# Optimization experiments

Measured on AMD Instinct MI355X. Metric: run time of the kernel, lower is better.

## Reference

```python
import jax, jax.numpy as jnp
import numpy as np

B, T, C_EMBD, C_ATT = 16, 1024, 2048, 2048


def wkv(time_decay, time_first, k, v):
    """Numerically-stable RWKV WKV recurrence (matches wkv_cuda).
    time_decay/time_first: [C]; k, v: [B, T, C] -> y: [B, T, C]."""
    w = -jnp.exp(time_decay)  # [C], decay is -exp(param)
    u = time_first
    Bn, Tn, Cn = k.shape

    def step(carry, kv_t):
        aa, bb, pp = carry          # each [B, C]
        kt, vt = kv_t               # [B, C]
        ww = u + kt
        p = jnp.maximum(pp, ww)
        e1 = jnp.exp(pp - p)
        e2 = jnp.exp(ww - p)
        y = (e1 * aa + e2 * vt) / (e1 * bb + e2)
        ww2 = pp + w
        p2 = jnp.maximum(ww2, kt)
        e1b = jnp.exp(ww2 - p2)
        e2b = jnp.exp(kt - p2)
        new = (e1b * aa + e2b * vt, e1b * bb + e2b, p2)
        return new, y

    init = (jnp.zeros((Bn, Cn), k.dtype),
            jnp.zeros((Bn, Cn), k.dtype),
            jnp.full((Bn, Cn), -1e38, k.dtype))
    kT = jnp.swapaxes(k, 0, 1)  # [T, B, C]
    vT = jnp.swapaxes(v, 0, 1)
    _, ys = jax.lax.scan(step, init, (kT, vT))
    return jnp.swapaxes(ys, 0, 1)  # [B, T, C]


def setup_inputs() -> dict:
    key = jax.random.key(0)
    ks = jax.random.split(key, 10)
    xav = np.sqrt(2.0 / (C_EMBD + C_ATT))
    inp = {
        "x": jax.random.normal(ks[0], (B, T, C_EMBD), jnp.float32),
        "time_decay": jax.random.normal(ks[1], (C_ATT,), jnp.float32) * 0.02,
        "time_first": jax.random.normal(ks[2], (C_ATT,), jnp.float32) * 0.02,
        "time_mix_k": jax.random.normal(ks[3], (1, 1, C_EMBD), jnp.float32) * 0.02,
        "time_mix_v": jax.random.normal(ks[4], (1, 1, C_EMBD), jnp.float32) * 0.02,
        "time_mix_r": jax.random.normal(ks[5], (1, 1, C_EMBD), jnp.float32) * 0.02,
        "key_w": jax.random.normal(ks[6], (C_ATT, C_EMBD), jnp.float32) * xav,
        "value_w": jax.random.normal(ks[7], (C_ATT, C_EMBD), jnp.float32) * xav,
        "receptance_w": jax.random.normal(ks[8], (C_ATT, C_EMBD), jnp.float32) * xav,
        "output_w": jax.random.normal(ks[9], (C_EMBD, C_ATT), jnp.float32) * xav,
    }
    return inp


def reference(x, time_decay, time_first, time_mix_k, time_mix_v, time_mix_r,
              key_w, value_w, receptance_w, output_w):
    # time shift: xx[:, t] = x[:, t-1], xx[:, 0] = 0
    xx = jnp.pad(x, ((0, 0), (1, 0), (0, 0)))[:, :-1]
    xk = x * time_mix_k + xx * (1 - time_mix_k)
    xv = x * time_mix_v + xx * (1 - time_mix_v)
    xr = x * time_mix_r + xx * (1 - time_mix_r)
    k = jnp.einsum('btc,dc->btd', xk, key_w)
    v = jnp.einsum('btc,dc->btd', xv, value_w)
    r = jnp.einsum('btc,dc->btd', xr, receptance_w)
    sr = jax.nn.sigmoid(r)
    rwkv = sr * wkv(time_decay, time_first, k, v)
    return jnp.einsum('btd,cd->btc', rwkv, output_w)
```

## Files before the change

### kernel.cpp

```cpp
#include <hip/hip_runtime.h>
#include <hip/hip_bf16.h>

#define BB 16
#define TT 1024
#define CC 2048
#define TS 32

typedef __attribute__((ext_vector_type(4))) float f32x4;
typedef __attribute__((ext_vector_type(8))) short bf16x8;

__device__ __forceinline__ unsigned short f2bf(float f) {
  union { float f; unsigned u; } x; x.f = f;
  unsigned r = x.u + 0x7fffu + ((x.u >> 16) & 1u);
  return (unsigned short)(r >> 16);
}
__device__ __forceinline__ float bf2f(unsigned short u) {
  union { unsigned u; float f; } x; x.u = ((unsigned)u) << 16;
  return x.f;
}

__device__ __forceinline__ ushort4 mix4(float4 a, float4 b, float4 m) {
  ushort4 o;
  o.x = f2bf(a.x * m.x + b.x * (1.f - m.x));
  o.y = f2bf(a.y * m.y + b.y * (1.f - m.y));
  o.z = f2bf(a.z * m.z + b.z * (1.f - m.z));
  o.w = f2bf(a.w * m.w + b.w * (1.f - m.w));
  return o;
}

__global__ void f2bf_all(const float* __restrict__ w0, const float* __restrict__ w1,
                         const float* __restrict__ w2, const float* __restrict__ w3,
                         unsigned short* __restrict__ o0, unsigned short* __restrict__ o1,
                         unsigned short* __restrict__ o2, unsigned short* __restrict__ o3,
                         int n4each) {
  const float* ws[4] = {w0, w1, w2, w3};
  unsigned short* os[4] = {o0, o1, o2, o3};
  int total = 4 * n4each;
  for (int i = blockIdx.x * blockDim.x + threadIdx.x; i < total;
       i += gridDim.x * blockDim.x) {
    int seg = i / n4each, j = i - seg * n4each;
    float4 v = ((const float4*)ws[seg])[j];
    ushort4 o;
    o.x = f2bf(v.x); o.y = f2bf(v.y); o.z = f2bf(v.z); o.w = f2bf(v.w);
    ((ushort4*)os[seg])[j] = o;
  }
}

__global__ void mix_kernel(const float* __restrict__ x,
                           const float* __restrict__ tmk,
                           const float* __restrict__ tmv,
                           const float* __restrict__ tmr,
                           unsigned short* __restrict__ xk,
                           unsigned short* __restrict__ xv,
                           unsigned short* __restrict__ xr,
                           int t0, int Tc) {
  const int C4 = CC / 4;
  const int total = BB * Tc * C4;
  for (int g = blockIdx.x * blockDim.x + threadIdx.x; g < total;
       g += gridDim.x * blockDim.x) {
    int cg = g % C4;
    int lrow = g / C4;
    int tl = lrow % Tc;
    int b = lrow / Tc;
    int t = t0 + tl;
    size_t gidx = (size_t)(b * TT + t) * C4 + cg;
    float4 xc = ((const float4*)x)[gidx];
    float4 xp = make_float4(0.f, 0.f, 0.f, 0.f);
    if (t > 0) xp = ((const float4*)x)[gidx - C4];
    ((ushort4*)xk)[g] = mix4(xc, xp, ((const float4*)tmk)[cg]);
    ((ushort4*)xv)[g] = mix4(xc, xp, ((const float4*)tmv)[cg]);
    ((ushort4*)xr)[g] = mix4(xc, xp, ((const float4*)tmr)[cg]);
  }
}

template<bool BF16OUT>
__global__ __launch_bounds__(512, 2)
void gemm256(const unsigned short* __restrict__ A,
             const unsigned short* __restrict__ B,
             void* __restrict__ Cv, int M, int N, int K,
             int tcShift, int t0) {
  __shared__ __align__(1024) unsigned char lds[131072];
  const int tid = threadIdx.x;
  const int lane = tid & 63;
  const int wid = tid >> 6;
  const int wr = wid >> 2;
  const int wc = wid & 3;

  const int nwg = gridDim.x;
  const int cpx = nwg >> 3;
  const int bid = blockIdx.x;
  const int wg = (bid & 7) * cpx + (bid >> 3);
  const int bcolN = N >> 8;
  const int brow = wg / bcolN;
  const int bcol = wg % bcolN;

  const unsigned short* Ag = A + (size_t)(brow * 256) * K;
  const unsigned short* Bg = B + (size_t)(bcol * 256) * K;

  const int srow = tid >> 3;
  const int scolB = ((tid & 7) * 16) ^ ((srow & 7) << 4);
  const int scolE = scolB >> 1;
  const int ldsWave = wid * 1024;

#define STAGE(gbase, rowOff, ldsOff, kOff)                                     \
  __builtin_amdgcn_global_load_lds(                                            \
      (const __attribute__((address_space(1))) void*)(                         \
          (gbase) + (size_t)((rowOff) + srow) * K + (kOff) + scolE),           \
      (__attribute__((address_space(3))) void*)(lds + (ldsOff) + ldsWave),     \
      16, 0, 0)

  const int frow = lane & 15;
  const int fhi = (lane >> 4) << 4;

#define FRAG(tb, row, kk)                                                      \
  (*(const bf16x8*)(lds + (tb) + (row) * 128 +                                 \
                    ((((kk) << 6) + fhi) ^ (((row) & 7) << 4))))

#define FENCE asm volatile("" ::: "memory")

  const int NT = K >> 6;

  STAGE(Bg,   0, 32768 +     0, 0);
  STAGE(Bg,  64, 32768 +  8192, 0);
  STAGE(Bg, 128, 32768 + 16384, 0);
  STAGE(Bg, 192, 32768 + 24576, 0);
  STAGE(Ag,   0,             0, 0);
  STAGE(Ag, 128,         16384, 0);
  STAGE(Ag,  64,          8192, 0);
  STAGE(Ag, 192,         24576, 0);

  f32x4 acc[8][4] = {};
  bf16x8 af0[8], af1[8], bf0[4], bf1[4];

  asm volatile("s_waitcnt vmcnt(2)" ::: "memory");
  __builtin_amdgcn_s_barrier();
#pragma unroll
  for (int m = 0; m < 4; ++m)
#pragma unroll
    for (int kk = 0; kk < 2; ++kk)
      af0[m * 2 + kk] = FRAG(0, wr * 128 + m * 16 + frow, kk);
#pragma unroll
  for (int n = 0; n < 2; ++n)
#pragma unroll
    for (int kk = 0; kk < 2; ++kk)
      bf0[n * 2 + kk] = FRAG(32768, wc * 64 + n * 16 + frow, kk);

  for (int kt = 0; kt < NT; ++kt) {
    const int cur = (kt & 1) << 16;
    const int nxt = ((kt + 1) & 1) << 16;
    const int kN = (kt + 1) << 6;
    const bool st = (kt + 1 < NT);

    if (st) { STAGE(Bg, 0, nxt + 32768, kN); STAGE(Bg, 64, nxt + 32768 + 8192, kN); }
    __builtin_amdgcn_s_setprio(1);
#pragma unroll
    for (int m = 0; m < 4; ++m)
#pragma unroll
      for (int n = 0; n < 2; ++n)
#pragma unroll
        for (int kk = 0; kk < 2; ++kk)
          acc[m][n] = __builtin_amdgcn_mfma_f32_16x16x32_bf16(
              af0[m * 2 + kk], bf0[n * 2 + kk], acc[m][n], 0, 0, 0);
    __builtin_amdgcn_s_setprio(0);
#pragma unroll
    for (int n = 0; n < 2; ++n)
#pragma unroll
      for (int kk = 0; kk < 2; ++kk)
        bf1[n * 2 + kk] = FRAG(cur + 32768, wc * 64 + 32 + n * 16 + frow, kk);
    FENCE;
    if (st) { asm volatile("s_waitcnt vmcnt(2)" ::: "memory"); }
    else    { asm volatile("s_waitcnt vmcnt(0)" ::: "memory"); }
    __builtin_amdgcn_s_barrier();

    if (st) { STAGE(Bg, 128, nxt + 32768 + 16384, kN); STAGE(Bg, 192, nxt + 32768 + 24576, kN); }
#pragma unroll
    for (int m = 0; m < 4; ++m)
#pragma unroll
      for (int kk = 0; kk < 2; ++kk)
        af1[m * 2 + kk] = FRAG(cur, wr * 128 + 64 + m * 16 + frow, kk);
    __builtin_amdgcn_s_setprio(1);
#pragma unroll
    for (int m = 0; m < 4; ++m)
#pragma unroll
      for (int n = 0; n < 2; ++n)
#pragma unroll
        for (int kk = 0; kk < 2; ++kk)
          acc[m][2 + n] = __builtin_amdgcn_mfma_f32_16x16x32_bf16(
              af0[m * 2 + kk], bf1[n * 2 + kk], acc[m][2 + n], 0, 0, 0);
    __builtin_amdgcn_s_setprio(0);
    FENCE;
    __builtin_amdgcn_s_barrier();

    if (st) { STAGE(Ag, 0, nxt, kN); STAGE(Ag, 128, nxt + 16384, kN); }
    __builtin_amdgcn_s_setprio(1);
#pragma unroll
    for (int m = 0; m < 4; ++m)
#pragma unroll
      for (int n = 0; n < 2; ++n)
#pragma unroll
        for (int kk = 0; kk < 2; ++kk)
          acc[4 + m][2 + n] = __builtin_amdgcn_mfma_f32_16x16x32_bf16(
              af1[m * 2 + kk], bf1[n * 2 + kk], acc[4 + m][2 + n], 0, 0, 0);
    __builtin_amdgcn_s_setprio(0);
    FENCE;
    __builtin_amdgcn_s_barrier();

    if (st) { STAGE(Ag, 64, nxt + 8192, kN); STAGE(Ag, 192, nxt + 24576, kN); }
    __builtin_amdgcn_s_setprio(1);
#pragma unroll
    for (int m = 0; m < 4; ++m)
#pragma unroll
      for (int n = 0; n < 2; ++n)
#pragma unroll
        for (int kk = 0; kk < 2; ++kk)
          acc[4 + m][n] = __builtin_amdgcn_mfma_f32_16x16x32_bf16(
              af1[m * 2 + kk], bf0[n * 2 + kk], acc[4 + m][n], 0, 0, 0);
    __builtin_amdgcn_s_setprio(0);
    if (st) {
      asm volatile("s_waitcnt vmcnt(2)" ::: "memory");
      __builtin_amdgcn_s_barrier();
#pragma unroll
      for (int m = 0; m < 4; ++m)
#pragma unroll
        for (int kk = 0; kk < 2; ++kk)
          af0[m * 2 + kk] = FRAG(nxt, wr * 128 + m * 16 + frow, kk);
#pragma unroll
      for (int n = 0; n < 2; ++n)
#pragma unroll
        for (int kk = 0; kk < 2; ++kk)
          bf0[n * 2 + kk] = FRAG(nxt + 32768, wc * 64 + n * 16 + frow, kk);
      FENCE;
    }
  }
#undef STAGE
#undef FRAG
#undef FENCE

  const int crow0 = (lane >> 4) << 2;
  const int ccol = lane & 15;
  const int tcMask = (1 << tcShift) - 1;
#pragma unroll
  for (int am = 0; am < 8; ++am)
#pragma unroll
    for (int an = 0; an < 4; ++an) {
      const int col = bcol * 256 + wc * 64 + (an >> 1) * 32 + (an & 1) * 16 + ccol;
#pragma unroll
      for (int j = 0; j < 4; ++j) {
        int r = brow * 256 + wr * 128 + (am >> 2) * 64 + (am & 3) * 16 + crow0 + j;
        int orow = ((r >> tcShift) << 10) + t0 + (r & tcMask);
        if (BF16OUT)
          ((unsigned short*)Cv)[(size_t)orow * N + col] = f2bf(acc[am][an][j]);
        else
          ((float*)Cv)[(size_t)orow * N + col] = acc[am][an][j];
      }
    }
}

__global__ void wkv_part(const float* __restrict__ time_decay,
                         const unsigned short* __restrict__ k,
                         const unsigned short* __restrict__ v,
                         float* __restrict__ paA, float* __restrict__ paB,
                         float* __restrict__ paP, int Tc) {
  int idx = blockIdx.x * blockDim.x + threadIdx.x;
  int c = idx & (CC - 1);
  int b = (idx >> 11) & (BB - 1);
  int s = idx >> 15;
  float w = -__expf(time_decay[c]);
  float aa = 0.f, bb = 0.f, pp = -1e38f;
  size_t base = ((size_t)b * Tc + s * TS) * CC + c;
  for (int t = 0; t < TS; ++t) {
    size_t off = base + (size_t)t * CC;
    float kt = bf2f(k[off]), vt = bf2f(v[off]);
    float ww2 = pp + w;
    float p2 = fmaxf(ww2, kt);
    float e1 = __expf(ww2 - p2), e2 = __expf(kt - p2);
    aa = e1 * aa + e2 * vt;
    bb = e1 * bb + e2;
    pp = p2;
  }
  paA[idx] = aa; paB[idx] = bb; paP[idx] = pp;
}

__global__ void wkv_comb(const float* __restrict__ time_decay,
                         const float* __restrict__ paA,
                         const float* __restrict__ paB,
                         const float* __restrict__ paP,
                         float* __restrict__ inA, float* __restrict__ inB,
                         float* __restrict__ inP,
                         float* __restrict__ state, int S, int t0) {
  int idx = blockIdx.x * blockDim.x + threadIdx.x;
  int c = idx & (CC - 1);
  float w = -__expf(time_decay[c]);
  float wTs = w * (float)TS;
  float A, Bv, P;
  if (t0 == 0) { A = 0.f; Bv = 0.f; P = -1e38f; }
  else { A = state[idx]; Bv = state[32768 + idx]; P = state[65536 + idx]; }
  for (int s = 0; s < S; ++s) {
    size_t o = (size_t)s * 32768 + idx;
    inA[o] = A; inB[o] = Bv; inP[o] = P;
    float Pd = P + wTs;
    float Ps = paP[o];
    float Pn = fmaxf(Pd, Ps);
    float e1 = __expf(Pd - Pn), e2 = __expf(Ps - Pn);
    A = e1 * A + e2 * paA[o];
    Bv = e1 * Bv + e2 * paB[o];
    P = Pn;
  }
  state[idx] = A; state[32768 + idx] = Bv; state[65536 + idx] = P;
}

__global__ void wkv_out(const float* __restrict__ time_decay,
                        const float* __restrict__ time_first,
                        const unsigned short* __restrict__ k,
                        const unsigned short* __restrict__ v,
                        const unsigned short* __restrict__ r,
                        unsigned short* __restrict__ rwkv,
                        const float* __restrict__ inA,
                        const float* __restrict__ inB,
                        const float* __restrict__ inP, int Tc) {
  int idx = blockIdx.x * blockDim.x + threadIdx.x;
  int c = idx & (CC - 1);
  int b = (idx >> 11) & (BB - 1);
  int s = idx >> 15;
  float w = -__expf(time_decay[c]);
  float u = time_first[c];
  float aa = inA[idx], bb = inB[idx], pp = inP[idx];
  size_t base = ((size_t)b * Tc + s * TS) * CC + c;
  for (int t = 0; t < TS; ++t) {
    size_t off = base + (size_t)t * CC;
    float kt = bf2f(k[off]), vt = bf2f(v[off]);
    float ww = u + kt;
    float p = fmaxf(pp, ww);
    float e1 = __expf(pp - p), e2 = __expf(ww - p);
    float y = (e1 * aa + e2 * vt) / (e1 * bb + e2);
    float rr = bf2f(r[off]);
    float sr = 1.f / (1.f + __expf(-rr));
    rwkv[off] = f2bf(sr * y);
    float ww2 = pp + w;
    float p2 = fmaxf(ww2, kt);
    float e1b = __expf(ww2 - p2), e2b = __expf(kt - p2);
    aa = e1b * aa + e2b * vt;
    bb = e1b * bb + e2b;
    pp = p2;
  }
}

extern "C" void kernel_launch(void* const* d_in, const int* in_sizes, int n_in,
                              void* d_out, int out_size, void* d_ws,
                              size_t ws_size, hipStream_t stream) {
  const float* x          = (const float*)d_in[0];
  const float* time_decay = (const float*)d_in[1];
  const float* time_first = (const float*)d_in[2];
  const float* tmk        = (const float*)d_in[3];
  const float* tmv        = (const float*)d_in[4];
  const float* tmr        = (const float*)d_in[5];
  const float* key_w      = (const float*)d_in[6];
  const float* value_w    = (const float*)d_in[7];
  const float* rec_w      = (const float*)d_in[8];
  const float* out_w      = (const float*)d_in[9];
  float* out = (float*)d_out;

  const size_t WW = (size_t)CC * CC;
  const size_t wtBytes = 4 * WW * 2;
  const size_t stBytes = 3 * (size_t)BB * CC * 4;

  int Tc = 1024;
  while (Tc > 32) {
    size_t chunkBytes = (size_t)BB * Tc * CC * 12;
    if (wtBytes + stBytes + chunkBytes + 1024 <= ws_size) break;
    Tc >>= 1;
  }
  const int Mc = BB * Tc;
  const size_t NC = (size_t)Mc * CC;
  const int S = Tc / TS;

  char* p = (char*)d_ws;
  unsigned short* wk  = (unsigned short*)p; p += WW * 2;
  unsigned short* wv  = (unsigned short*)p; p += WW * 2;
  unsigned short* wrr = (unsigned short*)p; p += WW * 2;
  unsigned short* wo  = (unsigned short*)p; p += WW * 2;
  float* state        = (float*)p;          p += stBytes;
  unsigned short* kbuf= (unsigned short*)p; p += NC * 2;
  unsigned short* vbuf= (unsigned short*)p; p += NC * 2;
  unsigned short* xk  = (unsigned short*)p; p += NC * 2;
  unsigned short* xv  = (unsigned short*)p; p += NC * 2;
  unsigned short* xr  = (unsigned short*)p; p += NC * 2;
  unsigned short* rbuf= (unsigned short*)p; p += NC * 2;
  unsigned short* rwkv = xk;

  const size_t SBt = (size_t)S * 32768;
  float* paA = (float*)xv;
  float* paB = paA + SBt;
  float* paP = paB + SBt;
  float* inA = paP + SBt;
  float* inB = inA + SBt;
  float* inP = inB + SBt;

  f2bf_all<<<2048, 256, 0, stream>>>(key_w, value_w, rec_w, out_w,
                                     wk, wv, wrr, wo, (int)(WW / 4));

  int tcShift = 0;
  while ((1 << tcShift) < Tc) ++tcShift;

  const int nwg = (Mc / 256) * (CC / 256);
  int mixBlocks = (Mc * (CC / 4) + 255) / 256;
  if (mixBlocks > 4096) mixBlocks = 4096;

  for (int t0 = 0; t0 < TT; t0 += Tc) {
    mix_kernel<<<mixBlocks, 256, 0, stream>>>(x, tmk, tmv, tmr, xk, xv, xr,
                                              t0, Tc);
    gemm256<true><<<nwg, 512, 0, stream>>>(xk, wk, kbuf, Mc, CC, CC, 10, 0);
    gemm256<true><<<nwg, 512, 0, stream>>>(xv, wv, vbuf, Mc, CC, CC, 10, 0);
    wkv_part<<<S * 128, 256, 0, stream>>>(time_decay, kbuf, vbuf,
                                          paA, paB, paP, Tc);
    gemm256<true><<<nwg, 512, 0, stream>>>(xr, wrr, rbuf, Mc, CC, CC, 10, 0);
    wkv_comb<<<128, 256, 0, stream>>>(time_decay, paA, paB, paP,
                                      inA, inB, inP, state, S, t0);
    wkv_out<<<S * 128, 256, 0, stream>>>(time_decay, time_first, kbuf, vbuf,
                                         rbuf, rwkv, inA, inB, inP, Tc);
    gemm256<false><<<nwg, 512, 0, stream>>>(rwkv, wo, out, Mc, CC, CC,
                                            tcShift, t0);
  }
}
```

Measured before the change: 728.1 us.

## Restructure GEMM main loop into 8-phase ping-pong schedule with half-tile LDS staging

Replaces the 4-phase-per-K-tile GEMM loop with an 8-phase loop over two K tiles. A and B are split into half-tiles in separate LDS regions, and global-to-LDS loads are interleaved per half-tile alongside MFMA quadrants, with barriers around each compute block. The aim is finer-grained overlap of global loads with MFMA and smaller register fragment sets (one af and one bf buffer instead of two each). It adds more barriers per K step and a more complex wait-count scheme, with the risk of sync stalls or ordering bugs.

```diff
diff --git a/kernel.cpp b/kernel.cpp
--- a/kernel.cpp
+++ b/kernel.cpp
@@ -98,143 +98,120 @@
   const unsigned short* Bg = B + (size_t)(bcol * 256) * K;
 
   const int srow = tid >> 3;
-  const int scolB = ((tid & 7) * 16) ^ ((srow & 7) << 4);
-  const int scolE = scolB >> 1;
+  const int scolE = ((((tid & 7) * 16) ^ ((srow & 7) << 4)) >> 1);
   const int ldsWave = wid * 1024;
-
-#define STAGE(gbase, rowOff, ldsOff, kOff)                                     \
+  const int rowB0 = ((srow >> 5) << 6) + (srow & 31);
+
+  const int frow = lane & 15;
+  const int fhi = (lane >> 4) << 4;
+  const int fsw = (frow & 7) << 4;
+
+#define STA(par, h, g, kk)                                                     \
   __builtin_amdgcn_global_load_lds(                                            \
       (const __attribute__((address_space(1))) void*)(                         \
-          (gbase) + (size_t)((rowOff) + srow) * K + (kOff) + scolE),           \
-      (__attribute__((address_space(3))) void*)(lds + (ldsOff) + ldsWave),     \
+          Ag + (size_t)(srow + (h) * 64 + (g) * 128) * K + (kk) + scolE),      \
+      (__attribute__((address_space(3))) void*)(                               \
+          lds + (par) * 32768 + (h) * 16384 + (g) * 8192 + ldsWave), 16, 0, 0)
+#define STB(par, h, g, kk)                                                     \
+  __builtin_amdgcn_global_load_lds(                                            \
+      (const __attribute__((address_space(1))) void*)(                         \
+          Bg + (size_t)(rowB0 + (h) * 32 + (g) * 128) * K + (kk) + scolE),     \
+      (__attribute__((address_space(3))) void*)(                               \
+          lds + 65536 + (par) * 32768 + (h) * 16384 + (g) * 8192 + ldsWave),   \
       16, 0, 0)
 
-  const int frow = lane & 15;
-  const int fhi = (lane >> 4) << 4;
-
-#define FRAG(tb, row, kk)                                                      \
-  (*(const bf16x8*)(lds + (tb) + (row) * 128 +                                 \
-                    ((((kk) << 6) + fhi) ^ (((row) & 7) << 4))))
-
-#define FENCE asm volatile("" ::: "memory")
-
-  const int NT = K >> 6;
-
-  STAGE(Bg,   0, 32768 +     0, 0);
-  STAGE(Bg,  64, 32768 +  8192, 0);
-  STAGE(Bg, 128, 32768 + 16384, 0);
-  STAGE(Bg, 192, 32768 + 24576, 0);
-  STAGE(Ag,   0,             0, 0);
-  STAGE(Ag, 128,         16384, 0);
-  STAGE(Ag,  64,          8192, 0);
-  STAGE(Ag, 192,         24576, 0);
+#define RD_A(par, h)                                                           \
+  do { _Pragma("unroll") for (int m = 0; m < 4; ++m)                           \
+       _Pragma("unroll") for (int kk = 0; kk < 2; ++kk)                        \
+         af[m * 2 + kk] = *(const bf16x8*)(lds + (par) * 32768 +               \
+             (h) * 16384 + (wr * 64 + m * 16 + frow) * 128 +                   \
+             (((kk << 6) + fhi) ^ fsw));                                       \
+  } while (0)
+#define RD_B(par, h)                                                           \
+  do { _Pragma("unroll") for (int n = 0; n < 2; ++n)                           \
+       _Pragma("unroll") for (int kk = 0; kk < 2; ++kk)                        \
+         bf[n * 2 + kk] = *(const bf16x8*)(lds + 65536 + (par) * 32768 +       \
+             (h) * 16384 + (wc * 32 + n * 16 + frow) * 128 +                   \
+             (((kk << 6) + fhi) ^ fsw));                                       \
+  } while (0)
+
+#define MFMA_Q(AM, AN)                                                         \
+  do { __builtin_amdgcn_s_setprio(1);                                          \
+       _Pragma("unroll") for (int m = 0; m < 4; ++m)                           \
+       _Pragma("unroll") for (int n = 0; n < 2; ++n)                           \
+       _Pragma("unroll") for (int kk = 0; kk < 2; ++kk)                        \
+         acc[(AM) + m][(AN) + n] = __builtin_amdgcn_mfma_f32_16x16x32_bf16(    \
+             af[m * 2 + kk], bf[n * 2 + kk], acc[(AM) + m][(AN) + n], 0, 0, 0);\
+       __builtin_amdgcn_s_setprio(0); } while (0)
+
+#define BAR __builtin_amdgcn_s_barrier()
+#define VMC4 asm volatile("s_waitcnt vmcnt(4)" ::: "memory")
+#define VMC0 asm volatile("s_waitcnt vmcnt(0)" ::: "memory")
+
+  const int NI = K >> 7;
+
+  STA(0, 0, 0, 0); STA(0, 0, 1, 0);
+  STA(0, 1, 0, 0); STA(0, 1, 1, 0);
+  STB(0, 0, 0, 0); STB(0, 0, 1, 0);
+  STB(0, 1, 0, 0); STB(0, 1, 1, 0);
+  STA(1, 0, 0, 64); STA(1, 0, 1, 64);
+  STB(1, 1, 0, 64); STB(1, 1, 1, 64);
+  VMC4;
+  BAR;
 
   f32x4 acc[8][4] = {};
-  bf16x8 af0[8], af1[8], bf0[4], bf1[4];
-
-  asm volatile("s_waitcnt vmcnt(2)" ::: "memory");
-  __builtin_amdgcn_s_barrier();
-#pragma unroll
-  for (int m = 0; m < 4; ++m)
-#pragma unroll
-    for (int kk = 0; kk < 2; ++kk)
-      af0[m * 2 + kk] = FRAG(0, wr * 128 + m * 16 + frow, kk);
-#pragma unroll
-  for (int n = 0; n < 2; ++n)
-#pragma unroll
-    for (int kk = 0; kk < 2; ++kk)
-      bf0[n * 2 + kk] = FRAG(32768, wc * 64 + n * 16 + frow, kk);
-
-  for (int kt = 0; kt < NT; ++kt) {
-    const int cur = (kt & 1) << 16;
-    const int nxt = ((kt + 1) & 1) << 16;
-    const int kN = (kt + 1) << 6;
-    const bool st = (kt + 1 < NT);
-
-    if (st) { STAGE(Bg, 0, nxt + 32768, kN); STAGE(Bg, 64, nxt + 32768 + 8192, kN); }
-    __builtin_amdgcn_s_setprio(1);
-#pragma unroll
-    for (int m = 0; m < 4; ++m)
-#pragma unroll
-      for (int n = 0; n < 2; ++n)
-#pragma unroll
-        for (int kk = 0; kk < 2; ++kk)
-          acc[m][n] = __builtin_amdgcn_mfma_f32_16x16x32_bf16(
-              af0[m * 2 + kk], bf0[n * 2 + kk], acc[m][n], 0, 0, 0);
-    __builtin_amdgcn_s_setprio(0);
-#pragma unroll
-    for (int n = 0; n < 2; ++n)
-#pragma unroll
-      for (int kk = 0; kk < 2; ++kk)
-        bf1[n * 2 + kk] = FRAG(cur + 32768, wc * 64 + 32 + n * 16 + frow, kk);
-    FENCE;
-    if (st) { asm volatile("s_waitcnt vmcnt(2)" ::: "memory"); }
-    else    { asm volatile("s_waitcnt vmcnt(0)" ::: "memory"); }
-    __builtin_amdgcn_s_barrier();
-
-    if (st) { STAGE(Bg, 128, nxt + 32768 + 16384, kN); STAGE(Bg, 192, nxt + 32768 + 24576, kN); }
-#pragma unroll
-    for (int m = 0; m < 4; ++m)
-#pragma unroll
-      for (int kk = 0; kk < 2; ++kk)
-        af1[m * 2 + kk] = FRAG(cur, wr * 128 + 64 + m * 16 + frow, kk);
-    __builtin_amdgcn_s_setprio(1);
-#pragma unroll
-    for (int m = 0; m < 4; ++m)
-#pragma unroll
-      for (int n = 0; n < 2; ++n)
-#pragma unroll
-        for (int kk = 0; kk < 2; ++kk)
-          acc[m][2 + n] = __builtin_amdgcn_mfma_f32_16x16x32_bf16(
-              af0[m * 2 + kk], bf1[n * 2 + kk], acc[m][2 + n], 0, 0, 0);
-    __builtin_amdgcn_s_setprio(0);
-    FENCE;
-    __builtin_amdgcn_s_barrier();
-
-    if (st) { STAGE(Ag, 0, nxt, kN); STAGE(Ag, 128, nxt + 16384, kN); }
-    __builtin_amdgcn_s_setprio(1);
-#pragma unroll
-    for (int m = 0; m < 4; ++m)
-#pragma unroll
-      for (int n = 0; n < 2; ++n)
-#pragma unroll
-        for (int kk = 0; kk < 2; ++kk)
-          acc[4 + m][2 + n] = __builtin_amdgcn_mfma_f32_16x16x32_bf16(
-              af1[m * 2 + kk], bf1[n * 2 + kk], acc[4 + m][2 + n], 0, 0, 0);
-    __builtin_amdgcn_s_setprio(0);
-    FENCE;
-    __builtin_amdgcn_s_barrier();
-
-    if (st) { STAGE(Ag, 64, nxt + 8192, kN); STAGE(Ag, 192, nxt + 24576, kN); }
-    __builtin_amdgcn_s_setprio(1);
-#pragma unroll
-    for (int m = 0; m < 4; ++m)
-#pragma unroll
-      for (int n = 0; n < 2; ++n)
-#pragma unroll
-        for (int kk = 0; kk < 2; ++kk)
-          acc[4 + m][n] = __builtin_amdgcn_mfma_f32_16x16x32_bf16(
-              af1[m * 2 + kk], bf0[n * 2 + kk], acc[4 + m][n], 0, 0, 0);
-    __builtin_amdgcn_s_setprio(0);
-    if (st) {
-      asm volatile("s_waitcnt vmcnt(2)" ::: "memory");
-      __builtin_amdgcn_s_barrier();
-#pragma unroll
-      for (int m = 0; m < 4; ++m)
-#pragma unroll
-        for (int kk = 0; kk < 2; ++kk)
-          af0[m * 2 + kk] = FRAG(nxt, wr * 128 + m * 16 + frow, kk);
-#pragma unroll
-      for (int n = 0; n < 2; ++n)
-#pragma unroll
-        for (int kk = 0; kk < 2; ++kk)
-          bf0[n * 2 + kk] = FRAG(nxt + 32768, wc * 64 + n * 16 + frow, kk);
-      FENCE;
-    }
-  }
-#undef STAGE
-#undef FRAG
-#undef FENCE
+  bf16x8 af[8], bf[4];
+
+  for (int i = 0; i < NI; ++i) {
+    const int k1 = (2 * i + 1) << 6;
+    const int k2 = (2 * i + 2) << 6;
+    const int k3 = (2 * i + 3) << 6;
+    const bool st = (i + 1 < NI);
+
+    RD_A(0, 0); RD_B(0, 0);
+    STB(1, 0, 0, k1); STB(1, 0, 1, k1);
+    BAR; MFMA_Q(0, 0); BAR;
+
+    RD_B(0, 1);
+    STA(1, 1, 0, k1); STA(1, 1, 1, k1);
+    BAR; MFMA_Q(0, 2); BAR;
+
+    RD_A(0, 1);
+    if (st) { STA(0, 0, 0, k2); STA(0, 0, 1, k2); }
+    BAR; MFMA_Q(4, 2); BAR;
+
+    RD_B(0, 0);
+    if (st) { STB(0, 1, 0, k2); STB(0, 1, 1, k2); }
+    BAR; MFMA_Q(4, 0);
+    if (st) { VMC4; } else { VMC0; }
+    BAR;
+
+    RD_A(1, 0); RD_B(1, 0);
+    if (st) { STA(0, 1, 0, k2); STA(0, 1, 1, k2); }
+    BAR; MFMA_Q(0, 0); BAR;
+
+    RD_B(1, 1);
+    if (st) { STB(0, 0, 0, k2); STB(0, 0, 1, k2); }
+    BAR; MFMA_Q(0, 2); BAR;
+
+    RD_A(1, 1);
+    if (st) { STA(1, 0, 0, k3); STA(1, 0, 1, k3); }
+    BAR; MFMA_Q(4, 2); BAR;
+
+    RD_B(1, 0);
+    if (st) { STB(1, 1, 0, k3); STB(1, 1, 1, k3); }
+    BAR; MFMA_Q(4, 0);
+    if (st) { VMC4; }
+    BAR;
+  }
+#undef STA
+#undef STB
+#undef RD_A
+#undef RD_B
+#undef MFMA_Q
+#undef BAR
+#undef VMC4
+#undef VMC0
 
   const int crow0 = (lane >> 4) << 2;
   const int ccol = lane & 15;
```

Measured after the change: 715.4 us. Within noise of the previous version (-1.7%).
